# Performance work log

Measured on AMD Instinct MI355X. Metric: run time of the kernel, lower is better.

The kernel has to match this reference:

```python
import jax, jax.numpy as jnp
import numpy as np

B, T, D, H, C = 64, 1024, 128, 512, 2


def setup_inputs() -> dict:
    key = jax.random.key(0)
    ks = jax.random.split(key, 6)
    x = jax.random.normal(ks[0], (B, T, D), dtype=jnp.float32)
    labels = jax.random.randint(ks[1], (B, T), 0, C, dtype=jnp.int32)
    # Keras LSTMCell params: kernel [D,4H], recurrent_kernel [H,4H], bias [4H]
    Wx = jax.random.normal(ks[2], (D, 4 * H), dtype=jnp.float32) * (1.0 / np.sqrt(D))
    Wh = jax.random.normal(ks[3], (H, 4 * H), dtype=jnp.float32) * (1.0 / np.sqrt(H))
    b = jnp.zeros((4 * H,), dtype=jnp.float32).at[H:2 * H].set(1.0)  # unit forget bias
    Wo = jax.random.normal(ks[4], (H, C), dtype=jnp.float32) * (1.0 / np.sqrt(H))
    bo = jnp.zeros((C,), dtype=jnp.float32)
    return {"x": x, "labels": labels, "Wx": Wx, "Wh": Wh, "b": b, "Wo": Wo, "bo": bo}


def _lstm_logits(x, Wx, Wh, b, Wo, bo):
    # Precompute input contribution for all steps: [B,T,4H]
    xz = jnp.einsum('btd,dk->btk', x, Wx) + b

    def step(carry, z_t):
        h, c = carry
        z = z_t + h @ Wh                     # [B,4H]
        i, f, g, o = jnp.split(z, 4, axis=-1)  # keras gate order: i,f,c,o
        i = jax.nn.sigmoid(i)
        f = jax.nn.sigmoid(f)
        g = jnp.tanh(g)
        o = jax.nn.sigmoid(o)
        c = f * c + i * g
        h = o * jnp.tanh(c)
        return (h, c), h

    h0 = jnp.zeros((x.shape[0], Wh.shape[0]), dtype=x.dtype)
    (_, _), hs = jax.lax.scan(step, (h0, h0), jnp.swapaxes(xz, 0, 1))
    hs = jnp.swapaxes(hs, 0, 1)              # [B,T,H]
    return jnp.einsum('bth,hc->btc', hs, Wo) + bo  # [B,T,C]


def reference(x, labels, Wx, Wh, b, Wo, bo):
    logits = _lstm_logits(x, Wx, Wh, b, Wo, bo)
    logp = jax.nn.log_softmax(logits, axis=-1)
    prediction = jnp.exp(logp)               # softmax probs
    nll = -jnp.take_along_axis(logp, labels[..., None].astype(jnp.int32), axis=-1)[..., 0]
    cost = jnp.mean(nll)
    return prediction, cost
```

## Files before the change

### kernel.cpp

```cpp
#include <hip/hip_runtime.h>
#include <stdint.h>

#define TLEN 1024
#define BATCH 64
#define DIMX 128
#define HID 512

typedef __attribute__((ext_vector_type(8))) short short8;
typedef __attribute__((ext_vector_type(4))) float f32x4;
typedef __attribute__((ext_vector_type(4))) unsigned u32x4;

#define OFF_WT   0u
#define OFF_XBF  2621440u
#define OFF_HB   19398656u
#define OFF_ACC  19660800u
#define ZERO_LEN (262144u + 64u)

__device__ __forceinline__ unsigned short f2bf(float f) {
  unsigned u = __float_as_uint(f);
  u += 0x7fffu + ((u >> 16) & 1u);
  return (unsigned short)(u >> 16);
}
__device__ __forceinline__ float sigm(float x) { return 1.0f / (1.0f + __expf(-x)); }
__device__ __forceinline__ float tanh_fast(float x) {
  float a = fabsf(x);
  float e = __expf(2.0f * a);
  float t = 1.0f - 2.0f / (e + 1.0f);
  return copysignf(t, x);
}

__global__ void k_convx(const float4* __restrict__ x4, ushort4* __restrict__ o4) {
  int i = blockIdx.x * 256 + threadIdx.x;
  float4 v = x4[i];
  ushort4 o;
  o.x = f2bf(v.x); o.y = f2bf(v.y); o.z = f2bf(v.z); o.w = f2bf(v.w);
  o4[i] = o;
}

__global__ void k_tw(const float* __restrict__ Wx, const float* __restrict__ Wh,
                     unsigned short* __restrict__ Wt) {
  __shared__ float tile[32][65];
  int bk = blockIdx.x;
  int k0 = (bk / 64) * 64;
  int c0 = (bk % 64) * 32;
  int tid = threadIdx.x;
  const float* src = (k0 < 128) ? (Wx + (size_t)k0 * 2048)
                                : (Wh + (size_t)(k0 - 128) * 2048);
#pragma unroll
  for (int p = 0; p < 8; ++p) {
    int i = p * 256 + tid;
    int kk = i >> 5, cc = i & 31;
    tile[cc][kk] = src[(size_t)kk * 2048 + (c0 + cc)];
  }
  __syncthreads();
  int cc = tid >> 3, ch = tid & 7;
  unsigned short tmp[8];
#pragma unroll
  for (int j = 0; j < 8; ++j) tmp[j] = f2bf(tile[cc][ch * 8 + j]);
  uint4 o;
  o.x = (unsigned)tmp[0] | ((unsigned)tmp[1] << 16);
  o.y = (unsigned)tmp[2] | ((unsigned)tmp[3] << 16);
  o.z = (unsigned)tmp[4] | ((unsigned)tmp[5] << 16);
  o.w = (unsigned)tmp[6] | ((unsigned)tmp[7] << 16);
  *(uint4*)(Wt + (size_t)(c0 + cc) * 640 + k0 + ch * 8) = o;
}

__global__ __launch_bounds__(512, 1) void k_lstm(
    const unsigned short* __restrict__ xbf,
    const unsigned short* __restrict__ Wt,
    const float* __restrict__ bias,
    const float* __restrict__ Wo,
    unsigned* __restrict__ hb,
    float* __restrict__ out)
{
  __shared__ float red[2][4][4][8][32];
  __shared__ short8 xch[2][4][2][2][64];
  __shared__ unsigned xflag[2][4][2];

  const int tid  = threadIdx.x;
  const int w    = tid >> 6;
  const int kw   = w & 3;
  const int cg   = w >> 2;
  const int lane = tid & 63;
  const int q    = lane >> 4;
  const int m    = lane & 15;
  const int grp  = blockIdx.x & 7;
  const int hj   = blockIdx.x >> 3;
  const int g0   = grp * 8;

  if (tid < 16) xflag[tid >> 3][(tid >> 1) & 3][tid & 1] = 0;

  short8 Bf[5][4];
#pragma unroll
  for (int cc = 0; cc < 5; ++cc) {
#pragma unroll
    for (int j = 0; j < 4; ++j) {
      int gate = cg * 2 + (j >> 1);
      int col = gate * HID + hj * 32 + (j & 1) * 16 + m;
      int k = (cc == 0) ? (kw * 32 + q * 8)
                        : (128 + kw * 128 + (cc - 1) * 32 + q * 8);
      Bf[cc][j] = *(const short8*)(Wt + (size_t)col * 640 + k);
    }
  }

  const int col  = lane & 31;
  const int hcol = hj * 32 + col;
  float c_state = 0.0f;
  const float b_i = bias[0 * HID + hcol];
  const float b_f = bias[1 * HID + hcol];
  const float b_g = bias[2 * HID + hcol];
  const float b_o = bias[3 * HID + hcol];
  const float2 wo = ((const float2*)Wo)[hcol];

  const int arow = (m < 8) ? m : 7;
  const int ab = g0 + arow;

  __syncthreads();

#pragma unroll 1
  for (int t = 0; t < TLEN; ++t) {
    const unsigned* hin = hb + (size_t)(t & 1) * (BATCH * HID);
    const int buf = t & 1;

    short8 a0 = *(const short8*)(xbf + ((size_t)ab * TLEN + t) * DIMX +
                                 kw * 32 + q * 8);

    const unsigned* pb = hin + (size_t)ab * HID + kw * 128 + cg * 64 + q * 8;
    u32x4 r0, r1, r2, r3;
    {
      const unsigned tg = (unsigned)t & 0xFFFFu;
      int guard = 0;
      for (;;) {
        asm volatile(
            "global_load_dwordx4 %0, %4, off sc0 sc1\n\t"
            "global_load_dwordx4 %1, %4, off offset:16 sc0 sc1\n\t"
            "global_load_dwordx4 %2, %4, off offset:128 sc0 sc1\n\t"
            "global_load_dwordx4 %3, %4, off offset:144 sc0 sc1\n\t"
            "s_waitcnt vmcnt(0)"
            : "=v"(r0), "=v"(r1), "=v"(r2), "=v"(r3)
            : "v"(pb)
            : "memory");
        unsigned d = (r0[0] ^ tg) | (r0[1] ^ tg) | (r0[2] ^ tg) | (r0[3] ^ tg);
        d |= (r1[0] ^ tg) | (r1[1] ^ tg) | (r1[2] ^ tg) | (r1[3] ^ tg);
        d |= (r2[0] ^ tg) | (r2[1] ^ tg) | (r2[2] ^ tg) | (r2[3] ^ tg);
        d |= (r3[0] ^ tg) | (r3[1] ^ tg) | (r3[2] ^ tg) | (r3[3] ^ tg);
        bool bad = (d & 0xFFFFu) != 0u;
        if (__ballot(bad) == 0ull || ++guard > (1 << 20)) break;
      }
    }

    short8 f0, f1;
    {
      union { short8 s; unsigned u[4]; } pk;
      pk.u[0] = (r0[0] >> 16) | (r0[1] & 0xFFFF0000u);
      pk.u[1] = (r0[2] >> 16) | (r0[3] & 0xFFFF0000u);
      pk.u[2] = (r1[0] >> 16) | (r1[1] & 0xFFFF0000u);
      pk.u[3] = (r1[2] >> 16) | (r1[3] & 0xFFFF0000u);
      f0 = pk.s;
      pk.u[0] = (r2[0] >> 16) | (r2[1] & 0xFFFF0000u);
      pk.u[1] = (r2[2] >> 16) | (r2[3] & 0xFFFF0000u);
      pk.u[2] = (r3[0] >> 16) | (r3[1] & 0xFFFF0000u);
      pk.u[3] = (r3[2] >> 16) | (r3[3] & 0xFFFF0000u);
      f1 = pk.s;
    }

    xch[buf][kw][cg][0][lane] = f0;
    xch[buf][kw][cg][1][lane] = f1;
    __hip_atomic_store(&xflag[buf][kw][cg], (unsigned)(t + 1),
                       __ATOMIC_RELEASE, __HIP_MEMORY_SCOPE_WORKGROUP);
    {
      int guard = 0;
      while (__hip_atomic_load(&xflag[buf][kw][cg ^ 1], __ATOMIC_ACQUIRE,
                               __HIP_MEMORY_SCOPE_WORKGROUP) < (unsigned)(t + 1)) {
        if (++guard > (1 << 22)) break;
      }
    }
    short8 s0 = xch[buf][kw][cg ^ 1][0][lane];
    short8 s1 = xch[buf][kw][cg ^ 1][1][lane];

    short8 a1 = cg ? s0 : f0;
    short8 a2 = cg ? s1 : f1;
    short8 a3 = cg ? f0 : s0;
    short8 a4 = cg ? f1 : s1;

    f32x4 z0 = {0,0,0,0}, z1 = {0,0,0,0}, z2 = {0,0,0,0}, z3 = {0,0,0,0};
    z0 = __builtin_amdgcn_mfma_f32_16x16x32_bf16(a0, Bf[0][0], z0, 0, 0, 0);
    z1 = __builtin_amdgcn_mfma_f32_16x16x32_bf16(a0, Bf[0][1], z1, 0, 0, 0);
    z2 = __builtin_amdgcn_mfma_f32_16x16x32_bf16(a0, Bf[0][2], z2, 0, 0, 0);
    z3 = __builtin_amdgcn_mfma_f32_16x16x32_bf16(a0, Bf[0][3], z3, 0, 0, 0);
    z0 = __builtin_amdgcn_mfma_f32_16x16x32_bf16(a1, Bf[1][0], z0, 0, 0, 0);
    z1 = __builtin_amdgcn_mfma_f32_16x16x32_bf16(a1, Bf[1][1], z1, 0, 0, 0);
    z2 = __builtin_amdgcn_mfma_f32_16x16x32_bf16(a1, Bf[1][2], z2, 0, 0, 0);
    z3 = __builtin_amdgcn_mfma_f32_16x16x32_bf16(a1, Bf[1][3], z3, 0, 0, 0);
    z0 = __builtin_amdgcn_mfma_f32_16x16x32_bf16(a2, Bf[2][0], z0, 0, 0, 0);
    z1 = __builtin_amdgcn_mfma_f32_16x16x32_bf16(a2, Bf[2][1], z1, 0, 0, 0);
    z2 = __builtin_amdgcn_mfma_f32_16x16x32_bf16(a2, Bf[2][2], z2, 0, 0, 0);
    z3 = __builtin_amdgcn_mfma_f32_16x16x32_bf16(a2, Bf[2][3], z3, 0, 0, 0);
    z0 = __builtin_amdgcn_mfma_f32_16x16x32_bf16(a3, Bf[3][0], z0, 0, 0, 0);
    z1 = __builtin_amdgcn_mfma_f32_16x16x32_bf16(a3, Bf[3][1], z1, 0, 0, 0);
    z2 = __builtin_amdgcn_mfma_f32_16x16x32_bf16(a3, Bf[3][2], z2, 0, 0, 0);
    z3 = __builtin_amdgcn_mfma_f32_16x16x32_bf16(a3, Bf[3][3], z3, 0, 0, 0);
    z0 = __builtin_amdgcn_mfma_f32_16x16x32_bf16(a4, Bf[4][0], z0, 0, 0, 0);
    z1 = __builtin_amdgcn_mfma_f32_16x16x32_bf16(a4, Bf[4][1], z1, 0, 0, 0);
    z2 = __builtin_amdgcn_mfma_f32_16x16x32_bf16(a4, Bf[4][2], z2, 0, 0, 0);
    z3 = __builtin_amdgcn_mfma_f32_16x16x32_bf16(a4, Bf[4][3], z3, 0, 0, 0);

    if (q < 2) {
#pragma unroll
      for (int r = 0; r < 4; ++r) {
        int rw = q * 4 + r;
        red[buf][kw][cg * 2 + 0][rw][0 * 16 + m] = z0[r];
        red[buf][kw][cg * 2 + 0][rw][1 * 16 + m] = z1[r];
        red[buf][kw][cg * 2 + 1][rw][0 * 16 + m] = z2[r];
        red[buf][kw][cg * 2 + 1][rw][1 * 16 + m] = z3[r];
      }
    }
    __syncthreads();

    if (lane < 32) {
      float zi = b_i + red[buf][0][0][w][col] + red[buf][1][0][w][col]
                     + red[buf][2][0][w][col] + red[buf][3][0][w][col];
      float zf = b_f + red[buf][0][1][w][col] + red[buf][1][1][w][col]
                     + red[buf][2][1][w][col] + red[buf][3][1][w][col];
      float zg = b_g + red[buf][0][2][w][col] + red[buf][1][2][w][col]
                     + red[buf][2][2][w][col] + red[buf][3][2][w][col];
      float zo = b_o + red[buf][0][3][w][col] + red[buf][1][3][w][col]
                     + red[buf][2][3][w][col] + red[buf][3][3][w][col];
      float ig = sigm(zi), fg = sigm(zf), gg = tanh_fast(zg), og = sigm(zo);
      c_state = fg * c_state + ig * gg;
      float hval = og * tanh_fast(c_state);

      unsigned hword = ((unsigned)f2bf(hval) << 16) | (unsigned)((t + 1) & 0xFFFF);
      int base = lane & ~3;
      unsigned w0 = __shfl(hword, base + 0);
      unsigned w1 = __shfl(hword, base + 1);
      unsigned w2 = __shfl(hword, base + 2);
      unsigned w3 = __shfl(hword, base + 3);
      if ((lane & 3) == 0) {
        u32x4 v4 = {w0, w1, w2, w3};
        unsigned* dst = hb + (size_t)((t + 1) & 1) * (BATCH * HID) +
                        (size_t)(g0 + w) * HID + hcol;
        asm volatile("global_store_dwordx4 %0, %1, off sc0 sc1"
                     :: "v"(dst), "v"(v4) : "memory");
      }

      float p0 = hval * wo.x, p1 = hval * wo.y;
      p0 += __shfl_xor(p0, 16); p1 += __shfl_xor(p1, 16);
      p0 += __shfl_xor(p0, 8);  p1 += __shfl_xor(p1, 8);
      p0 += __shfl_xor(p0, 4);  p1 += __shfl_xor(p1, 4);
      p0 += __shfl_xor(p0, 2);  p1 += __shfl_xor(p1, 2);
      p0 += __shfl_xor(p0, 1);  p1 += __shfl_xor(p1, 1);
      if (lane == 0) {
        float* po = out + ((size_t)(g0 + w) * TLEN + t) * 2;
        atomicAdd(po + 0, p0);
        atomicAdd(po + 1, p1);
      }
    }
  }
}

__global__ void k_out2(float* __restrict__ out, const float* __restrict__ bo,
                       const int* __restrict__ labels, float* __restrict__ acc) {
  __shared__ float sred[4];
  int i = blockIdx.x * 256 + threadIdx.x;
  float l0 = out[(size_t)i * 2 + 0] + bo[0];
  float l1 = out[(size_t)i * 2 + 1] + bo[1];
  float mx = fmaxf(l0, l1);
  float e0 = __expf(l0 - mx), e1 = __expf(l1 - mx);
  float s = e0 + e1, inv = 1.0f / s;
  out[(size_t)i * 2 + 0] = e0 * inv;
  out[(size_t)i * 2 + 1] = e1 * inv;
  int lab = labels[i];
  float nll = __logf(s) - ((lab ? l1 : l0) - mx);
#pragma unroll
  for (int off = 32; off >= 1; off >>= 1) nll += __shfl_xor(nll, off);
  if ((threadIdx.x & 63) == 0) sred[threadIdx.x >> 6] = nll;
  __syncthreads();
  if (threadIdx.x == 0)
    atomicAdd(acc, sred[0] + sred[1] + sred[2] + sred[3]);
}

__global__ void k_fin(const float* __restrict__ acc, float* __restrict__ out) {
  out[BATCH * TLEN * 2] = acc[0] * (1.0f / (float)(BATCH * TLEN));
}

extern "C" void kernel_launch(void* const* d_in, const int* in_sizes, int n_in,
                              void* d_out, int out_size, void* d_ws, size_t ws_size,
                              hipStream_t stream) {
  const float* x      = (const float*)d_in[0];
  const int*   labels = (const int*)d_in[1];
  const float* Wx     = (const float*)d_in[2];
  const float* Wh     = (const float*)d_in[3];
  const float* b      = (const float*)d_in[4];
  const float* Wo     = (const float*)d_in[5];
  const float* bo     = (const float*)d_in[6];
  float* out = (float*)d_out;
  char* ws = (char*)d_ws;

  unsigned short* Wt  = (unsigned short*)(ws + OFF_WT);
  unsigned short* xbf = (unsigned short*)(ws + OFF_XBF);
  unsigned*       hb  = (unsigned*)(ws + OFF_HB);
  float*          acc = (float*)(ws + OFF_ACC);

  hipMemsetAsync(ws + OFF_HB, 0, ZERO_LEN, stream);
  hipMemsetAsync(d_out, 0, (size_t)BATCH * TLEN * 2 * sizeof(float), stream);
  k_convx<<<8192, 256, 0, stream>>>((const float4*)x, (ushort4*)xbf);
  k_tw<<<640, 256, 0, stream>>>(Wx, Wh, Wt);
  k_lstm<<<128, 512, 0, stream>>>(xbf, Wt, b, Wo, hb, out);
  k_out2<<<256, 256, 0, stream>>>(out, bo, labels, acc);
  k_fin<<<1, 1, 0, stream>>>(acc, out);
}
```

Baseline: 2.811 ms.

## Use 32 larger LSTM blocks with full 16-row MFMA tiles and partial logits

The persistent LSTM kernel now runs on 32 workgroups instead of 128. Each covers 16 batch rows by 64 hidden columns, so the 16-row MFMA tiles are fully used instead of padding 8 rows, and fewer blocks take part in each cross-block handoff of the hidden state. The input-projection MFMAs are issued before the spin-wait on the previous hidden state, so they overlap the wait. Output logits become per-block partial sums written with plain stores and reduced in the softmax kernel, which removes the float atomics and the output memset. In exchange, each block holds twice the B-fragment registers and does twice the MFMA and gate work per step, with an added barrier after the reduction read.

```diff
diff --git a/kernel.cpp b/kernel.cpp
--- a/kernel.cpp
+++ b/kernel.cpp
@@ -14,7 +14,8 @@
 #define OFF_XBF  2621440u
 #define OFF_HB   19398656u
 #define OFF_ACC  19660800u
-#define ZERO_LEN (262144u + 64u)
+#define OFF_PART 19660864u
+#define ZERO_LEN 262208u
 
 __device__ __forceinline__ unsigned short f2bf(float f) {
   unsigned u = __float_as_uint(f);
@@ -27,6 +28,16 @@
   float e = __expf(2.0f * a);
   float t = 1.0f - 2.0f / (e + 1.0f);
   return copysignf(t, x);
+}
+
+__device__ __forceinline__ bool tags_bad(const u32x4& r0, const u32x4& r1,
+                                         const u32x4& r2, const u32x4& r3,
+                                         unsigned tg) {
+  unsigned d = (r0[0] ^ tg) | (r0[1] ^ tg) | (r0[2] ^ tg) | (r0[3] ^ tg);
+  d |= (r1[0] ^ tg) | (r1[1] ^ tg) | (r1[2] ^ tg) | (r1[3] ^ tg);
+  d |= (r2[0] ^ tg) | (r2[1] ^ tg) | (r2[2] ^ tg) | (r2[3] ^ tg);
+  d |= (r3[0] ^ tg) | (r3[1] ^ tg) | (r3[2] ^ tg) | (r3[3] ^ tg);
+  return (d & 0xFFFFu) != 0u;
 }
 
 __global__ void k_convx(const float4* __restrict__ x4, ushort4* __restrict__ o4) {
@@ -71,9 +82,9 @@
     const float* __restrict__ bias,
     const float* __restrict__ Wo,
     unsigned* __restrict__ hb,
-    float* __restrict__ out)
+    float* __restrict__ part)
 {
-  __shared__ float red[2][4][4][8][32];
+  __shared__ float red[4][4][16][64];
   __shared__ short8 xch[2][4][2][2][64];
   __shared__ unsigned xflag[2][4][2];
 
@@ -84,36 +95,37 @@
   const int lane = tid & 63;
   const int q    = lane >> 4;
   const int m    = lane & 15;
-  const int grp  = blockIdx.x & 7;
-  const int hj   = blockIdx.x >> 3;
-  const int g0   = grp * 8;
+  const int grp  = blockIdx.x & 3;
+  const int hj   = blockIdx.x >> 2;
+  const int g0   = grp * 16;
 
   if (tid < 16) xflag[tid >> 3][(tid >> 1) & 3][tid & 1] = 0;
 
-  short8 Bf[5][4];
+  short8 Bf[5][8];
 #pragma unroll
   for (int cc = 0; cc < 5; ++cc) {
 #pragma unroll
-    for (int j = 0; j < 4; ++j) {
-      int gate = cg * 2 + (j >> 1);
-      int col = gate * HID + hj * 32 + (j & 1) * 16 + m;
+    for (int j = 0; j < 8; ++j) {
+      int gate = cg * 2 + (j >> 2);
+      int col = gate * HID + hj * 64 + (j & 3) * 16 + m;
       int k = (cc == 0) ? (kw * 32 + q * 8)
                         : (128 + kw * 128 + (cc - 1) * 32 + q * 8);
       Bf[cc][j] = *(const short8*)(Wt + (size_t)col * 640 + k);
     }
   }
 
-  const int col  = lane & 31;
-  const int hcol = hj * 32 + col;
-  float c_state = 0.0f;
+  const int colx = lane;
+  const int hcol = hj * 64 + colx;
+  const int row0 = w * 2, row1 = w * 2 + 1;
+  float c0s = 0.0f, c1s = 0.0f;
   const float b_i = bias[0 * HID + hcol];
   const float b_f = bias[1 * HID + hcol];
   const float b_g = bias[2 * HID + hcol];
   const float b_o = bias[3 * HID + hcol];
   const float2 wo = ((const float2*)Wo)[hcol];
 
-  const int arow = (m < 8) ? m : 7;
-  const int ab = g0 + arow;
+  const int ab = g0 + m;
+  const size_t poff = (size_t)ab * HID + kw * 128 + cg * 64 + q * 8;
 
   __syncthreads();
 
@@ -124,8 +136,14 @@
 
     short8 a0 = *(const short8*)(xbf + ((size_t)ab * TLEN + t) * DIMX +
                                  kw * 32 + q * 8);
-
-    const unsigned* pb = hin + (size_t)ab * HID + kw * 128 + cg * 64 + q * 8;
+    f32x4 z[8];
+#pragma unroll
+    for (int j = 0; j < 8; ++j) z[j] = (f32x4){0.f, 0.f, 0.f, 0.f};
+#pragma unroll
+    for (int j = 0; j < 8; ++j)
+      z[j] = __builtin_amdgcn_mfma_f32_16x16x32_bf16(a0, Bf[0][j], z[j], 0, 0, 0);
+
+    const unsigned* pb = hin + poff;
     u32x4 r0, r1, r2, r3;
     {
       const unsigned tg = (unsigned)t & 0xFFFFu;
@@ -140,11 +158,7 @@
             : "=v"(r0), "=v"(r1), "=v"(r2), "=v"(r3)
             : "v"(pb)
             : "memory");
-        unsigned d = (r0[0] ^ tg) | (r0[1] ^ tg) | (r0[2] ^ tg) | (r0[3] ^ tg);
-        d |= (r1[0] ^ tg) | (r1[1] ^ tg) | (r1[2] ^ tg) | (r1[3] ^ tg);
-        d |= (r2[0] ^ tg) | (r2[1] ^ tg) | (r2[2] ^ tg) | (r2[3] ^ tg);
-        d |= (r3[0] ^ tg) | (r3[1] ^ tg) | (r3[2] ^ tg) | (r3[3] ^ tg);
-        bool bad = (d & 0xFFFFu) != 0u;
+        bool bad = tags_bad(r0, r1, r2, r3, tg);
         if (__ballot(bad) == 0ull || ++guard > (1 << 20)) break;
       }
     }
@@ -183,88 +197,95 @@
     short8 a3 = cg ? f0 : s0;
     short8 a4 = cg ? f1 : s1;
 
-    f32x4 z0 = {0,0,0,0}, z1 = {0,0,0,0}, z2 = {0,0,0,0}, z3 = {0,0,0,0};
-    z0 = __builtin_amdgcn_mfma_f32_16x16x32_bf16(a0, Bf[0][0], z0, 0, 0, 0);
-    z1 = __builtin_amdgcn_mfma_f32_16x16x32_bf16(a0, Bf[0][1], z1, 0, 0, 0);
-    z2 = __builtin_amdgcn_mfma_f32_16x16x32_bf16(a0, Bf[0][2], z2, 0, 0, 0);
-    z3 = __builtin_amdgcn_mfma_f32_16x16x32_bf16(a0, Bf[0][3], z3, 0, 0, 0);
-    z0 = __builtin_amdgcn_mfma_f32_16x16x32_bf16(a1, Bf[1][0], z0, 0, 0, 0);
-    z1 = __builtin_amdgcn_mfma_f32_16x16x32_bf16(a1, Bf[1][1], z1, 0, 0, 0);
-    z2 = __builtin_amdgcn_mfma_f32_16x16x32_bf16(a1, Bf[1][2], z2, 0, 0, 0);
-    z3 = __builtin_amdgcn_mfma_f32_16x16x32_bf16(a1, Bf[1][3], z3, 0, 0, 0);
-    z0 = __builtin_amdgcn_mfma_f32_16x16x32_bf16(a2, Bf[2][0], z0, 0, 0, 0);
-    z1 = __builtin_amdgcn_mfma_f32_16x16x32_bf16(a2, Bf[2][1], z1, 0, 0, 0);
-    z2 = __builtin_amdgcn_mfma_f32_16x16x32_bf16(a2, Bf[2][2], z2, 0, 0, 0);
-    z3 = __builtin_amdgcn_mfma_f32_16x16x32_bf16(a2, Bf[2][3], z3, 0, 0, 0);
-    z0 = __builtin_amdgcn_mfma_f32_16x16x32_bf16(a3, Bf[3][0], z0, 0, 0, 0);
-    z1 = __builtin_amdgcn_mfma_f32_16x16x32_bf16(a3, Bf[3][1], z1, 0, 0, 0);
-    z2 = __builtin_amdgcn_mfma_f32_16x16x32_bf16(a3, Bf[3][2], z2, 0, 0, 0);
-    z3 = __builtin_amdgcn_mfma_f32_16x16x32_bf16(a3, Bf[3][3], z3, 0, 0, 0);
-    z0 = __builtin_amdgcn_mfma_f32_16x16x32_bf16(a4, Bf[4][0], z0, 0, 0, 0);
-    z1 = __builtin_amdgcn_mfma_f32_16x16x32_bf16(a4, Bf[4][1], z1, 0, 0, 0);
-    z2 = __builtin_amdgcn_mfma_f32_16x16x32_bf16(a4, Bf[4][2], z2, 0, 0, 0);
-    z3 = __builtin_amdgcn_mfma_f32_16x16x32_bf16(a4, Bf[4][3], z3, 0, 0, 0);
-
-    if (q < 2) {
-#pragma unroll
-      for (int r = 0; r < 4; ++r) {
-        int rw = q * 4 + r;
-        red[buf][kw][cg * 2 + 0][rw][0 * 16 + m] = z0[r];
-        red[buf][kw][cg * 2 + 0][rw][1 * 16 + m] = z1[r];
-        red[buf][kw][cg * 2 + 1][rw][0 * 16 + m] = z2[r];
-        red[buf][kw][cg * 2 + 1][rw][1 * 16 + m] = z3[r];
-      }
+#pragma unroll
+    for (int j = 0; j < 8; ++j)
+      z[j] = __builtin_amdgcn_mfma_f32_16x16x32_bf16(a1, Bf[1][j], z[j], 0, 0, 0);
+#pragma unroll
+    for (int j = 0; j < 8; ++j)
+      z[j] = __builtin_amdgcn_mfma_f32_16x16x32_bf16(a2, Bf[2][j], z[j], 0, 0, 0);
+#pragma unroll
+    for (int j = 0; j < 8; ++j)
+      z[j] = __builtin_amdgcn_mfma_f32_16x16x32_bf16(a3, Bf[3][j], z[j], 0, 0, 0);
+#pragma unroll
+    for (int j = 0; j < 8; ++j)
+      z[j] = __builtin_amdgcn_mfma_f32_16x16x32_bf16(a4, Bf[4][j], z[j], 0, 0, 0);
+
+#pragma unroll
+    for (int j = 0; j < 8; ++j) {
+      int g = cg * 2 + (j >> 2);
+      int cb = (j & 3) * 16 + m;
+#pragma unroll
+      for (int r = 0; r < 4; ++r)
+        red[kw][g][q * 4 + r][cb] = z[j][r];
     }
     __syncthreads();
 
-    if (lane < 32) {
-      float zi = b_i + red[buf][0][0][w][col] + red[buf][1][0][w][col]
-                     + red[buf][2][0][w][col] + red[buf][3][0][w][col];
-      float zf = b_f + red[buf][0][1][w][col] + red[buf][1][1][w][col]
-                     + red[buf][2][1][w][col] + red[buf][3][1][w][col];
-      float zg = b_g + red[buf][0][2][w][col] + red[buf][1][2][w][col]
-                     + red[buf][2][2][w][col] + red[buf][3][2][w][col];
-      float zo = b_o + red[buf][0][3][w][col] + red[buf][1][3][w][col]
-                     + red[buf][2][3][w][col] + red[buf][3][3][w][col];
-      float ig = sigm(zi), fg = sigm(zf), gg = tanh_fast(zg), og = sigm(zo);
-      c_state = fg * c_state + ig * gg;
-      float hval = og * tanh_fast(c_state);
-
-      unsigned hword = ((unsigned)f2bf(hval) << 16) | (unsigned)((t + 1) & 0xFFFF);
-      int base = lane & ~3;
-      unsigned w0 = __shfl(hword, base + 0);
-      unsigned w1 = __shfl(hword, base + 1);
-      unsigned w2 = __shfl(hword, base + 2);
-      unsigned w3 = __shfl(hword, base + 3);
-      if ((lane & 3) == 0) {
-        u32x4 v4 = {w0, w1, w2, w3};
-        unsigned* dst = hb + (size_t)((t + 1) & 1) * (BATCH * HID) +
-                        (size_t)(g0 + w) * HID + hcol;
-        asm volatile("global_store_dwordx4 %0, %1, off sc0 sc1"
-                     :: "v"(dst), "v"(v4) : "memory");
-      }
-
-      float p0 = hval * wo.x, p1 = hval * wo.y;
-      p0 += __shfl_xor(p0, 16); p1 += __shfl_xor(p1, 16);
-      p0 += __shfl_xor(p0, 8);  p1 += __shfl_xor(p1, 8);
-      p0 += __shfl_xor(p0, 4);  p1 += __shfl_xor(p1, 4);
-      p0 += __shfl_xor(p0, 2);  p1 += __shfl_xor(p1, 2);
-      p0 += __shfl_xor(p0, 1);  p1 += __shfl_xor(p1, 1);
-      if (lane == 0) {
-        float* po = out + ((size_t)(g0 + w) * TLEN + t) * 2;
-        atomicAdd(po + 0, p0);
-        atomicAdd(po + 1, p1);
-      }
+    float zi0 = red[0][0][row0][colx] + red[1][0][row0][colx]
+              + red[2][0][row0][colx] + red[3][0][row0][colx];
+    float zf0 = red[0][1][row0][colx] + red[1][1][row0][colx]
+              + red[2][1][row0][colx] + red[3][1][row0][colx];
+    float zg0 = red[0][2][row0][colx] + red[1][2][row0][colx]
+              + red[2][2][row0][colx] + red[3][2][row0][colx];
+    float zo0 = red[0][3][row0][colx] + red[1][3][row0][colx]
+              + red[2][3][row0][colx] + red[3][3][row0][colx];
+    float zi1 = red[0][0][row1][colx] + red[1][0][row1][colx]
+              + red[2][0][row1][colx] + red[3][0][row1][colx];
+    float zf1 = red[0][1][row1][colx] + red[1][1][row1][colx]
+              + red[2][1][row1][colx] + red[3][1][row1][colx];
+    float zg1 = red[0][2][row1][colx] + red[1][2][row1][colx]
+              + red[2][2][row1][colx] + red[3][2][row1][colx];
+    float zo1 = red[0][3][row1][colx] + red[1][3][row1][colx]
+              + red[2][3][row1][colx] + red[3][3][row1][colx];
+    __syncthreads();
+
+    float ig0 = sigm(zi0 + b_i), fg0 = sigm(zf0 + b_f);
+    float gg0 = tanh_fast(zg0 + b_g), og0 = sigm(zo0 + b_o);
+    c0s = fg0 * c0s + ig0 * gg0;
+    float h0 = og0 * tanh_fast(c0s);
+    float ig1 = sigm(zi1 + b_i), fg1 = sigm(zf1 + b_f);
+    float gg1 = tanh_fast(zg1 + b_g), og1 = sigm(zo1 + b_o);
+    c1s = fg1 * c1s + ig1 * gg1;
+    float h1 = og1 * tanh_fast(c1s);
+
+    const unsigned tg1 = (unsigned)(t + 1) & 0xFFFFu;
+    unsigned hw0 = ((unsigned)f2bf(h0) << 16) | tg1;
+    unsigned hw1 = ((unsigned)f2bf(h1) << 16) | tg1;
+    unsigned* hob = hb + (size_t)((t + 1) & 1) * (BATCH * HID);
+    unsigned* d0 = hob + (size_t)(g0 + row0) * HID + hcol;
+    unsigned* d1 = hob + (size_t)(g0 + row1) * HID + hcol;
+    asm volatile("global_store_dword %0, %1, off sc0 sc1"
+                 :: "v"(d0), "v"(hw0) : "memory");
+    asm volatile("global_store_dword %0, %1, off sc0 sc1"
+                 :: "v"(d1), "v"(hw1) : "memory");
+
+    float p00 = h0 * wo.x, p01 = h0 * wo.y;
+    float p10 = h1 * wo.x, p11 = h1 * wo.y;
+#pragma unroll
+    for (int off = 32; off >= 1; off >>= 1) {
+      p00 += __shfl_xor(p00, off); p01 += __shfl_xor(p01, off);
+      p10 += __shfl_xor(p10, off); p11 += __shfl_xor(p11, off);
+    }
+    if (lane == 0) {
+      float2 v0; v0.x = p00; v0.y = p01;
+      float2 v1; v1.x = p10; v1.y = p11;
+      *(float2*)(part + (((size_t)hj * BATCH + (g0 + row0)) * TLEN + t) * 2) = v0;
+      *(float2*)(part + (((size_t)hj * BATCH + (g0 + row1)) * TLEN + t) * 2) = v1;
     }
   }
 }
 
 __global__ void k_out2(float* __restrict__ out, const float* __restrict__ bo,
-                       const int* __restrict__ labels, float* __restrict__ acc) {
+                       const int* __restrict__ labels,
+                       const float2* __restrict__ part,
+                       float* __restrict__ acc) {
   __shared__ float sred[4];
   int i = blockIdx.x * 256 + threadIdx.x;
-  float l0 = out[(size_t)i * 2 + 0] + bo[0];
-  float l1 = out[(size_t)i * 2 + 1] + bo[1];
+  float l0 = bo[0], l1 = bo[1];
+#pragma unroll
+  for (int hj = 0; hj < 8; ++hj) {
+    float2 p = part[(size_t)hj * (BATCH * TLEN) + i];
+    l0 += p.x; l1 += p.y;
+  }
   float mx = fmaxf(l0, l1);
   float e0 = __expf(l0 - mx), e1 = __expf(l1 - mx);
   float s = e0 + e1, inv = 1.0f / s;
@@ -301,12 +322,12 @@
   unsigned short* xbf = (unsigned short*)(ws + OFF_XBF);
   unsigned*       hb  = (unsigned*)(ws + OFF_HB);
   float*          acc = (float*)(ws + OFF_ACC);
+  float*          part = (float*)(ws + OFF_PART);
 
   hipMemsetAsync(ws + OFF_HB, 0, ZERO_LEN, stream);
-  hipMemsetAsync(d_out, 0, (size_t)BATCH * TLEN * 2 * sizeof(float), stream);
   k_convx<<<8192, 256, 0, stream>>>((const float4*)x, (ushort4*)xbf);
   k_tw<<<640, 256, 0, stream>>>(Wx, Wh, Wt);
-  k_lstm<<<128, 512, 0, stream>>>(xbf, Wt, b, Wo, hb, out);
-  k_out2<<<256, 256, 0, stream>>>(out, bo, labels, acc);
+  k_lstm<<<32, 512, 0, stream>>>(xbf, Wt, b, Wo, hb, part);
+  k_out2<<<256, 256, 0, stream>>>(out, bo, labels, (const float2*)part, acc);
   k_fin<<<1, 1, 0, stream>>>(acc, out);
 }
```

Result: slower. 4.018 ms (+42.9%).

## Hoist x-projection MFMAs before the spin-wait and replace output atomics with partials

Applied to the files above, without the earlier changes.

Issues the input-projection MFMAs before the global spin-wait on the hidden state, so they run while the block waits on other blocks. Each lane now stores its own tagged h dword, replacing the shuffle-gather and dwordx4 store. The per-step atomicAdd into the logits is replaced by plain float2 partial stores per hidden slice, which k_out2 sums over 16 slices. This also removes the output memset, at the cost of extra workspace and a reduction read in k_out2.

```diff
diff --git a/kernel.cpp b/kernel.cpp
--- a/kernel.cpp
+++ b/kernel.cpp
@@ -14,7 +14,8 @@
 #define OFF_XBF  2621440u
 #define OFF_HB   19398656u
 #define OFF_ACC  19660800u
-#define ZERO_LEN (262144u + 64u)
+#define OFF_PART 19660864u
+#define ZERO_LEN 262208u
 
 __device__ __forceinline__ unsigned short f2bf(float f) {
   unsigned u = __float_as_uint(f);
@@ -27,6 +28,16 @@
   float e = __expf(2.0f * a);
   float t = 1.0f - 2.0f / (e + 1.0f);
   return copysignf(t, x);
+}
+
+__device__ __forceinline__ bool tags_bad(const u32x4& r0, const u32x4& r1,
+                                         const u32x4& r2, const u32x4& r3,
+                                         unsigned tg) {
+  unsigned d = (r0[0] ^ tg) | (r0[1] ^ tg) | (r0[2] ^ tg) | (r0[3] ^ tg);
+  d |= (r1[0] ^ tg) | (r1[1] ^ tg) | (r1[2] ^ tg) | (r1[3] ^ tg);
+  d |= (r2[0] ^ tg) | (r2[1] ^ tg) | (r2[2] ^ tg) | (r2[3] ^ tg);
+  d |= (r3[0] ^ tg) | (r3[1] ^ tg) | (r3[2] ^ tg) | (r3[3] ^ tg);
+  return (d & 0xFFFFu) != 0u;
 }
 
 __global__ void k_convx(const float4* __restrict__ x4, ushort4* __restrict__ o4) {
@@ -71,7 +82,7 @@
     const float* __restrict__ bias,
     const float* __restrict__ Wo,
     unsigned* __restrict__ hb,
-    float* __restrict__ out)
+    float* __restrict__ part)
 {
   __shared__ float red[2][4][4][8][32];
   __shared__ short8 xch[2][4][2][2][64];
@@ -114,6 +125,7 @@
 
   const int arow = (m < 8) ? m : 7;
   const int ab = g0 + arow;
+  const size_t poff = (size_t)ab * HID + kw * 128 + cg * 64 + q * 8;
 
   __syncthreads();
 
@@ -124,8 +136,13 @@
 
     short8 a0 = *(const short8*)(xbf + ((size_t)ab * TLEN + t) * DIMX +
                                  kw * 32 + q * 8);
-
-    const unsigned* pb = hin + (size_t)ab * HID + kw * 128 + cg * 64 + q * 8;
+    f32x4 z0 = {0,0,0,0}, z1 = {0,0,0,0}, z2 = {0,0,0,0}, z3 = {0,0,0,0};
+    z0 = __builtin_amdgcn_mfma_f32_16x16x32_bf16(a0, Bf[0][0], z0, 0, 0, 0);
+    z1 = __builtin_amdgcn_mfma_f32_16x16x32_bf16(a0, Bf[0][1], z1, 0, 0, 0);
+    z2 = __builtin_amdgcn_mfma_f32_16x16x32_bf16(a0, Bf[0][2], z2, 0, 0, 0);
+    z3 = __builtin_amdgcn_mfma_f32_16x16x32_bf16(a0, Bf[0][3], z3, 0, 0, 0);
+
+    const unsigned* pb = hin + poff;
     u32x4 r0, r1, r2, r3;
     {
       const unsigned tg = (unsigned)t & 0xFFFFu;
@@ -140,11 +157,7 @@
             : "=v"(r0), "=v"(r1), "=v"(r2), "=v"(r3)
             : "v"(pb)
             : "memory");
-        unsigned d = (r0[0] ^ tg) | (r0[1] ^ tg) | (r0[2] ^ tg) | (r0[3] ^ tg);
-        d |= (r1[0] ^ tg) | (r1[1] ^ tg) | (r1[2] ^ tg) | (r1[3] ^ tg);
-        d |= (r2[0] ^ tg) | (r2[1] ^ tg) | (r2[2] ^ tg) | (r2[3] ^ tg);
-        d |= (r3[0] ^ tg) | (r3[1] ^ tg) | (r3[2] ^ tg) | (r3[3] ^ tg);
-        bool bad = (d & 0xFFFFu) != 0u;
+        bool bad = tags_bad(r0, r1, r2, r3, tg);
         if (__ballot(bad) == 0ull || ++guard > (1 << 20)) break;
       }
     }
@@ -183,11 +196,6 @@
     short8 a3 = cg ? f0 : s0;
     short8 a4 = cg ? f1 : s1;
 
-    f32x4 z0 = {0,0,0,0}, z1 = {0,0,0,0}, z2 = {0,0,0,0}, z3 = {0,0,0,0};
-    z0 = __builtin_amdgcn_mfma_f32_16x16x32_bf16(a0, Bf[0][0], z0, 0, 0, 0);
-    z1 = __builtin_amdgcn_mfma_f32_16x16x32_bf16(a0, Bf[0][1], z1, 0, 0, 0);
-    z2 = __builtin_amdgcn_mfma_f32_16x16x32_bf16(a0, Bf[0][2], z2, 0, 0, 0);
-    z3 = __builtin_amdgcn_mfma_f32_16x16x32_bf16(a0, Bf[0][3], z3, 0, 0, 0);
     z0 = __builtin_amdgcn_mfma_f32_16x16x32_bf16(a1, Bf[1][0], z0, 0, 0, 0);
     z1 = __builtin_amdgcn_mfma_f32_16x16x32_bf16(a1, Bf[1][1], z1, 0, 0, 0);
     z2 = __builtin_amdgcn_mfma_f32_16x16x32_bf16(a1, Bf[1][2], z2, 0, 0, 0);
@@ -231,18 +239,10 @@
       float hval = og * tanh_fast(c_state);
 
       unsigned hword = ((unsigned)f2bf(hval) << 16) | (unsigned)((t + 1) & 0xFFFF);
-      int base = lane & ~3;
-      unsigned w0 = __shfl(hword, base + 0);
-      unsigned w1 = __shfl(hword, base + 1);
-      unsigned w2 = __shfl(hword, base + 2);
-      unsigned w3 = __shfl(hword, base + 3);
-      if ((lane & 3) == 0) {
-        u32x4 v4 = {w0, w1, w2, w3};
-        unsigned* dst = hb + (size_t)((t + 1) & 1) * (BATCH * HID) +
-                        (size_t)(g0 + w) * HID + hcol;
-        asm volatile("global_store_dwordx4 %0, %1, off sc0 sc1"
-                     :: "v"(dst), "v"(v4) : "memory");
-      }
+      unsigned* dst = hb + (size_t)((t + 1) & 1) * (BATCH * HID) +
+                      (size_t)(g0 + w) * HID + hcol;
+      asm volatile("global_store_dword %0, %1, off sc0 sc1"
+                   :: "v"(dst), "v"(hword) : "memory");
 
       float p0 = hval * wo.x, p1 = hval * wo.y;
       p0 += __shfl_xor(p0, 16); p1 += __shfl_xor(p1, 16);
@@ -251,20 +251,25 @@
       p0 += __shfl_xor(p0, 2);  p1 += __shfl_xor(p1, 2);
       p0 += __shfl_xor(p0, 1);  p1 += __shfl_xor(p1, 1);
       if (lane == 0) {
-        float* po = out + ((size_t)(g0 + w) * TLEN + t) * 2;
-        atomicAdd(po + 0, p0);
-        atomicAdd(po + 1, p1);
+        float2 pv; pv.x = p0; pv.y = p1;
+        *(float2*)(part + (((size_t)hj * BATCH + (g0 + w)) * TLEN + t) * 2) = pv;
       }
     }
   }
 }
 
 __global__ void k_out2(float* __restrict__ out, const float* __restrict__ bo,
-                       const int* __restrict__ labels, float* __restrict__ acc) {
+                       const int* __restrict__ labels,
+                       const float2* __restrict__ part,
+                       float* __restrict__ acc) {
   __shared__ float sred[4];
   int i = blockIdx.x * 256 + threadIdx.x;
-  float l0 = out[(size_t)i * 2 + 0] + bo[0];
-  float l1 = out[(size_t)i * 2 + 1] + bo[1];
+  float l0 = bo[0], l1 = bo[1];
+#pragma unroll
+  for (int hj = 0; hj < 16; ++hj) {
+    float2 p = part[(size_t)hj * (BATCH * TLEN) + i];
+    l0 += p.x; l1 += p.y;
+  }
   float mx = fmaxf(l0, l1);
   float e0 = __expf(l0 - mx), e1 = __expf(l1 - mx);
   float s = e0 + e1, inv = 1.0f / s;
@@ -301,12 +306,12 @@
   unsigned short* xbf = (unsigned short*)(ws + OFF_XBF);
   unsigned*       hb  = (unsigned*)(ws + OFF_HB);
   float*          acc = (float*)(ws + OFF_ACC);
+  float*          part = (float*)(ws + OFF_PART);
 
   hipMemsetAsync(ws + OFF_HB, 0, ZERO_LEN, stream);
-  hipMemsetAsync(d_out, 0, (size_t)BATCH * TLEN * 2 * sizeof(float), stream);
   k_convx<<<8192, 256, 0, stream>>>((const float4*)x, (ushort4*)xbf);
   k_tw<<<640, 256, 0, stream>>>(Wx, Wh, Wt);
-  k_lstm<<<128, 512, 0, stream>>>(xbf, Wt, b, Wo, hb, out);
-  k_out2<<<256, 256, 0, stream>>>(out, bo, labels, acc);
+  k_lstm<<<128, 512, 0, stream>>>(xbf, Wt, b, Wo, hb, part);
+  k_out2<<<256, 256, 0, stream>>>(out, bo, labels, (const float2*)part, acc);
   k_fin<<<1, 1, 0, stream>>>(acc, out);
 }
```

Measured after the change: 2.900 ms. 1.03x slower.
